# Kernel optimization log

Hardware: AMD Instinct MI355X
Metric: run time of the kernel (lower is better)

## Reference

```python
import jax, jax.numpy as jnp
import numpy as np

H = 32        # hiddenSize
OUT = 256     # output_size
T = 60        # num_frames
EPS = 1e-5


def setup_inputs() -> dict:
    key = jax.random.key(0)
    ks = jax.random.split(key, 16)
    s = 0.05
    rn = lambda k, shp: (jax.random.normal(k, shp, dtype=jnp.float32) * s)
    return {
        "x": jax.random.normal(ks[0], (1, T, 63), dtype=jnp.float32),
        "w00": rn(ks[1], (63, 63)), "b00": rn(ks[2], (63,)),
        "w01": rn(ks[3], (64, 63)), "b01": rn(ks[4], (64,)),
        "ln_g": jnp.ones((64,), jnp.float32), "ln_b": jnp.zeros((64,), jnp.float32),
        "w_ih": rn(ks[5], (4 * H, 64)), "w_hh": rn(ks[6], (4 * H, H)),
        "b_ih": rn(ks[7], (4 * H,)), "b_hh": rn(ks[8], (4 * H,)),
        "bn_g": jnp.ones((H,), jnp.float32), "bn_b": jnp.zeros((H,), jnp.float32),
        "w10": rn(ks[9], (32, H)), "b10": rn(ks[10], (32,)),
        "w11": rn(ks[11], (32, 32)), "b11": rn(ks[12], (32,)),
        "w12": rn(ks[13], (OUT, 32)), "b12": rn(ks[14], (OUT,)),
    }


def _forward(x, w00, b00, w01, b01, ln_g, ln_b, w_ih, w_hh, b_ih, b_hh,
             bn_g, bn_b, w10, b10, w11, b11, w12, b12):
    # x: [1, T, 63] -> scan over T frames (fused MLP + LayerNorm + LSTM cell)
    xs = jnp.transpose(x, (1, 0, 2))  # [T, 1, 63]

    def step(carry, xt):  # xt: [1, 63]
        h, c = carry
        f = jax.nn.relu(xt @ w00.T + b00)          # [1, 63]
        f = jax.nn.relu(f @ w01.T + b01)           # [1, 64]
        mu = jnp.mean(f, axis=-1, keepdims=True)
        var = jnp.mean((f - mu) ** 2, axis=-1, keepdims=True)
        f = (f - mu) * jax.lax.rsqrt(var + EPS) * ln_g + ln_b
        gates = f @ w_ih.T + b_ih + h @ w_hh.T + b_hh  # [1, 4H]
        i_g, f_g, g_g, o_g = jnp.split(gates, 4, axis=-1)
        c = jax.nn.sigmoid(f_g) * c + jax.nn.sigmoid(i_g) * jnp.tanh(g_g)
        h = jax.nn.sigmoid(o_g) * jnp.tanh(c)
        return (h, c), None

    h0 = jnp.zeros((1, H), x.dtype)
    c0 = jnp.zeros((1, H), x.dtype)
    (h, _), _ = jax.lax.scan(step, (h0, c0), xs)
    # BatchNorm1d in eval mode (running_mean=0, running_var=1)
    out = h * jax.lax.rsqrt(jnp.float32(1.0) + EPS) * bn_g + bn_b
    out = jax.nn.relu(out @ w10.T + b10)
    out = jax.nn.relu(out @ w11.T + b11)
    return out @ w12.T + b12  # [1, OUT]


def reference(x, w00, b00, w01, b01, ln_g, ln_b, w_ih, w_hh, b_ih, b_hh,
              bn_g, bn_b, w10, b10, w11, b11, w12, b12):
    return _forward(x, w00, b00, w01, b01, ln_g, ln_b, w_ih, w_hh, b_ih, b_hh,
                    bn_g, bn_b, w10, b10, w11, b11, w12, b12)
```

## Files before the change

### kernel.cpp

```cpp
#include <hip/hip_runtime.h>

#define EPS 1e-5f
#define MAGIC 0x5CA9F1A6u

typedef __fp16 h2v2 __attribute__((ext_vector_type(2)));

__device__ __forceinline__ float frcp(float x) { return __builtin_amdgcn_rcpf(x); }
__device__ __forceinline__ float fsigm(float x) { return frcp(1.0f + __expf(-x)); }
__device__ __forceinline__ float ftanh(float x) {
    float e = __expf(-2.0f * x);
    return (1.0f - e) * frcp(1.0f + e);
}
__device__ __forceinline__ int rdli(int v, int k) {
    return __builtin_amdgcn_readlane(v, k);
}
__device__ __forceinline__ float rdl32(float v, int k) {
    return __int_as_float(__builtin_amdgcn_readlane(__float_as_int(v), 32 + k));
}
__device__ __forceinline__ float xhalf_sum(float x) {
#if __has_builtin(__builtin_amdgcn_permlane32_swap)
    auto r = __builtin_amdgcn_permlane32_swap(__float_as_uint(x),
                                              __float_as_uint(x), false, false);
    return __uint_as_float(r[0]) + __uint_as_float(r[1]);
#else
    return x + __shfl_xor(x, 32);
#endif
}
__device__ __forceinline__ float fdot2(h2v2 a, h2v2 b, float c) {
#if __has_builtin(__builtin_amdgcn_fdot2)
    return __builtin_amdgcn_fdot2(a, b, c, false);
#else
    return c + (float)a.x * (float)b.x + (float)a.y * (float)b.y;
#endif
}

__global__ __launch_bounds__(64) void fused_kernel(
    const float* __restrict__ x,
    const float* __restrict__ w00, const float* __restrict__ b00,
    const float* __restrict__ w01, const float* __restrict__ b01,
    const float* __restrict__ ln_g, const float* __restrict__ ln_b,
    const float* __restrict__ w_ih, const float* __restrict__ w_hh,
    const float* __restrict__ b_ih, const float* __restrict__ b_hh,
    const float* __restrict__ bn_g, const float* __restrict__ bn_b,
    const float* __restrict__ w10, const float* __restrict__ b10,
    const float* __restrict__ w11, const float* __restrict__ b11,
    const float* __restrict__ w12, const float* __restrict__ b12,
    float* __restrict__ Gx, unsigned* __restrict__ flags,
    float* __restrict__ out)
{
    __shared__ float scr[128];
    const int j = threadIdx.x;

    if (blockIdx.x < 60) {
        const int t = blockIdx.x;

        scr[j] = (j < 63) ? x[t * 63 + j] : 0.0f;
        __syncthreads();

        float f0 = 0.0f;
        if (j < 63) {
            const float* wr = w00 + j * 63;
            float acc = b00[j];
            #pragma unroll
            for (int k = 0; k < 63; k++) acc += scr[k] * wr[k];
            f0 = fmaxf(acc, 0.0f);
        }
        __syncthreads();
        scr[j] = f0;
        __syncthreads();

        float acc = b01[j];
        {
            const float* wr = w01 + j * 63;
            #pragma unroll
            for (int k = 0; k < 63; k++) acc += scr[k] * wr[k];
        }
        float f1 = fmaxf(acc, 0.0f);

        float s = f1, sq = f1 * f1;
        #pragma unroll
        for (int off = 32; off > 0; off >>= 1) {
            s  += __shfl_xor(s, off);
            sq += __shfl_xor(sq, off);
        }
        float mu  = s * (1.0f / 64.0f);
        float var = sq * (1.0f / 64.0f) - mu * mu;
        float f   = (f1 - mu) * rsqrtf(var + EPS) * ln_g[j] + ln_b[j];
        __syncthreads();
        scr[64 + j] = f;
        __syncthreads();

        float a0 = b_ih[j] + b_hh[j];
        float a1 = b_ih[j + 64] + b_hh[j + 64];
        const float* wi0 = w_ih + j * 64;
        const float* wi1 = w_ih + (j + 64) * 64;
        #pragma unroll
        for (int k = 0; k < 64; k++) {
            float fk = scr[64 + k];
            a0 += fk * wi0[k];
            a1 += fk * wi1[k];
        }
        Gx[t * 128 + j]      = a0;
        Gx[t * 128 + 64 + j] = a1;

        __threadfence();
        __syncthreads();
        if (j == 0)
            __hip_atomic_store(&flags[t], MAGIC, __ATOMIC_RELEASE,
                               __HIP_MEMORY_SCOPE_AGENT);
        return;
    }

    h2v2 wAh[16], wBh[16];
    {
        const float4* r0 = (const float4*)(w_hh + j * 32);
        const float4* r1 = (const float4*)(w_hh + (j + 64) * 32);
        #pragma unroll
        for (int q = 0; q < 8; q++) {
            float4 a = r0[q];
            float4 b = r1[q];
            wAh[2 * q + 0] = __builtin_amdgcn_cvt_pkrtz(a.x, a.y);
            wAh[2 * q + 1] = __builtin_amdgcn_cvt_pkrtz(a.z, a.w);
            wBh[2 * q + 0] = __builtin_amdgcn_cvt_pkrtz(b.x, b.y);
            wBh[2 * q + 1] = __builtin_amdgcn_cvt_pkrtz(b.z, b.w);
        }
    }

    {
        bool done = (j >= 60);
        while (true) {
            if (!done)
                done = (__hip_atomic_load(&flags[j], __ATOMIC_RELAXED,
                                          __HIP_MEMORY_SCOPE_AGENT) == MAGIC);
            if (__ballot(done) == ~0ULL) break;
            __builtin_amdgcn_s_sleep(1);
        }
        (void)__hip_atomic_load(&flags[0], __ATOMIC_ACQUIRE,
                                __HIP_MEMORY_SCOPE_AGENT);
    }

    const bool low = (j < 32);
    float c = 0.0f, hn = 0.0f;
    #pragma unroll 1
    for (int c0 = 0; c0 < 5; c0++) {
        float gAr[12], gBr[12];
        #pragma unroll
        for (int i = 0; i < 12; i++) {
            gAr[i] = Gx[(c0 * 12 + i) * 128 + j];
            gBr[i] = Gx[(c0 * 12 + i) * 128 + 64 + j];
        }
        #pragma unroll
        for (int i = 0; i < 12; i++) {
            int   hsw_i = __builtin_amdgcn_update_dpp(
                              0, __float_as_int(hn), 0xB1, 0xF, 0xF, true);
            h2v2  hpk   = __builtin_amdgcn_cvt_pkrtz(hn, __int_as_float(hsw_i));
            int   hpk_i = __builtin_bit_cast(int, hpk);

            int hh_i[16];
            #pragma unroll
            for (int k = 0; k < 16; k++) hh_i[k] = rdli(hpk_i, 32 + 2 * k);

            float aA0 = gAr[i], aA1 = 0.f, aA2 = 0.f, aA3 = 0.f;
            float aB0 = gBr[i], aB1 = 0.f, aB2 = 0.f, aB3 = 0.f;
            #pragma unroll
            for (int d = 0; d < 4; d++) {
                h2v2 h0 = __builtin_bit_cast(h2v2, hh_i[d]);
                h2v2 h1 = __builtin_bit_cast(h2v2, hh_i[4 + d]);
                h2v2 hx = __builtin_bit_cast(h2v2, hh_i[8 + d]);
                h2v2 h3 = __builtin_bit_cast(h2v2, hh_i[12 + d]);
                aA0 = fdot2(h0, wAh[d],      aA0);  aB0 = fdot2(h0, wBh[d],      aB0);
                aA1 = fdot2(h1, wAh[4 + d],  aA1);  aB1 = fdot2(h1, wBh[4 + d],  aB1);
                aA2 = fdot2(hx, wAh[8 + d],  aA2);  aB2 = fdot2(hx, wBh[8 + d],  aB2);
                aA3 = fdot2(h3, wAh[12 + d], aA3);  aB3 = fdot2(h3, wBh[12 + d], aB3);
            }
            float a0 = (aA0 + aA1) + (aA2 + aA3);
            float a1 = (aB0 + aB1) + (aB2 + aB3);

            float e1 = __expf(-a1);
            float sO = frcp(1.0f + e1);
            float e2 = e1 * e1;
            float t1 = (1.0f - e2) * frcp(1.0f + e2);
            float s0 = fsigm(a0);
            float own = s0 * (low ? t1 : c);
            c = xhalf_sum(own);
            hn = sO * ftanh(c);
        }
    }

    const float rs = rsqrtf(1.0f + EPS);
    const int ro = j & 31;
    float acc = b10[ro];
    #pragma unroll
    for (int k = 0; k < 32; k++) {
        float hkk = rdl32(hn, k);
        float hb = hkk * rs * bn_g[k] + bn_b[k];
        acc += w10[ro * 32 + k] * hb;
    }
    float o1 = fmaxf(acc, 0.0f);

    acc = b11[ro];
    #pragma unroll
    for (int k = 0; k < 32; k++)
        acc += w11[ro * 32 + k]
             * __int_as_float(__builtin_amdgcn_readlane(__float_as_int(o1), k));
    float o2 = fmaxf(acc, 0.0f);

    float a[4];
    #pragma unroll
    for (int r = 0; r < 4; r++) a[r] = b12[j + 64 * r];
    #pragma unroll
    for (int k = 0; k < 32; k++) {
        float hv = __int_as_float(__builtin_amdgcn_readlane(__float_as_int(o2), k));
        #pragma unroll
        for (int r = 0; r < 4; r++) a[r] += w12[(j + 64 * r) * 32 + k] * hv;
    }
    #pragma unroll
    for (int r = 0; r < 4; r++) out[j + 64 * r] = a[r];
}

extern "C" void kernel_launch(void* const* d_in, const int* in_sizes, int n_in,
                              void* d_out, int out_size, void* d_ws, size_t ws_size,
                              hipStream_t stream) {
    const float* x    = (const float*)d_in[0];
    const float* w00  = (const float*)d_in[1];
    const float* b00  = (const float*)d_in[2];
    const float* w01  = (const float*)d_in[3];
    const float* b01  = (const float*)d_in[4];
    const float* ln_g = (const float*)d_in[5];
    const float* ln_b = (const float*)d_in[6];
    const float* w_ih = (const float*)d_in[7];
    const float* w_hh = (const float*)d_in[8];
    const float* b_ih = (const float*)d_in[9];
    const float* b_hh = (const float*)d_in[10];
    const float* bn_g = (const float*)d_in[11];
    const float* bn_b = (const float*)d_in[12];
    const float* w10  = (const float*)d_in[13];
    const float* b10  = (const float*)d_in[14];
    const float* w11  = (const float*)d_in[15];
    const float* b11  = (const float*)d_in[16];
    const float* w12  = (const float*)d_in[17];
    const float* b12  = (const float*)d_in[18];
    float* out = (float*)d_out;
    float*    Gx    = (float*)d_ws;
    unsigned* flags = (unsigned*)((char*)d_ws + 49152);

    fused_kernel<<<61, 64, 0, stream>>>(x, w00, b00, w01, b01, ln_g, ln_b,
                                        w_ih, w_hh, b_ih, b_hh, bn_g, bn_b,
                                        w10, b10, w11, b11, w12, b12,
                                        Gx, flags, out);
}
```

Before: 109.0 us.

## Wait per 12-step chunk, prefetch head weights, fold log2e into gate preactivations

The recurrent block now waits only for the flags of the current 12-frame chunk instead of all 60, so the LSTM recurrence can start while producer blocks are still computing later frame projections. The head MLP weights and biases are preloaded into registers before the recurrence, taking their global loads off the tail of the kernel. Gate preactivations and recurrent weights are prescaled by log2(e) so sigmoid and tanh use exp2 directly, and the dot-product accumulation uses 8 independent chains. Costs are higher register pressure (about 160 extra floats per lane, which may spill) and fp16 rounding of the scaled weights.

```diff
diff --git a/kernel.cpp b/kernel.cpp
--- a/kernel.cpp
+++ b/kernel.cpp
@@ -2,14 +2,17 @@
 
 #define EPS 1e-5f
 #define MAGIC 0x5CA9F1A6u
+#define LOG2E 1.44269504f
 
 typedef __fp16 h2v2 __attribute__((ext_vector_type(2)));
 
 __device__ __forceinline__ float frcp(float x) { return __builtin_amdgcn_rcpf(x); }
-__device__ __forceinline__ float fsigm(float x) { return frcp(1.0f + __expf(-x)); }
-__device__ __forceinline__ float ftanh(float x) {
-    float e = __expf(-2.0f * x);
-    return (1.0f - e) * frcp(1.0f + e);
+__device__ __forceinline__ float fexp2(float x) {
+#if __has_builtin(__builtin_amdgcn_exp2f)
+    return __builtin_amdgcn_exp2f(x);
+#else
+    return exp2f(x);
+#endif
 }
 __device__ __forceinline__ int rdli(int v, int k) {
     return __builtin_amdgcn_readlane(v, k);
@@ -100,8 +103,8 @@
             a0 += fk * wi0[k];
             a1 += fk * wi1[k];
         }
-        Gx[t * 128 + j]      = a0;
-        Gx[t * 128 + 64 + j] = a1;
+        Gx[t * 128 + j]      = a0 * LOG2E;
+        Gx[t * 128 + 64 + j] = a1 * LOG2E;
 
         __threadfence();
         __syncthreads();
@@ -119,30 +122,59 @@
         for (int q = 0; q < 8; q++) {
             float4 a = r0[q];
             float4 b = r1[q];
-            wAh[2 * q + 0] = __builtin_amdgcn_cvt_pkrtz(a.x, a.y);
-            wAh[2 * q + 1] = __builtin_amdgcn_cvt_pkrtz(a.z, a.w);
-            wBh[2 * q + 0] = __builtin_amdgcn_cvt_pkrtz(b.x, b.y);
-            wBh[2 * q + 1] = __builtin_amdgcn_cvt_pkrtz(b.z, b.w);
-        }
-    }
-
+            wAh[2 * q + 0] = __builtin_amdgcn_cvt_pkrtz(a.x * LOG2E, a.y * LOG2E);
+            wAh[2 * q + 1] = __builtin_amdgcn_cvt_pkrtz(a.z * LOG2E, a.w * LOG2E);
+            wBh[2 * q + 0] = __builtin_amdgcn_cvt_pkrtz(b.x * LOG2E, b.y * LOG2E);
+            wBh[2 * q + 1] = __builtin_amdgcn_cvt_pkrtz(b.z * LOG2E, b.w * LOG2E);
+        }
+    }
+
+    const int ro = j & 31;
+    float w10r[32], w11r[32], w12r[4][32];
+    float b10r, b11r, b12r[4];
     {
-        bool done = (j >= 60);
-        while (true) {
-            if (!done)
-                done = (__hip_atomic_load(&flags[j], __ATOMIC_RELAXED,
-                                          __HIP_MEMORY_SCOPE_AGENT) == MAGIC);
-            if (__ballot(done) == ~0ULL) break;
-            __builtin_amdgcn_s_sleep(1);
-        }
-        (void)__hip_atomic_load(&flags[0], __ATOMIC_ACQUIRE,
-                                __HIP_MEMORY_SCOPE_AGENT);
-    }
+        const float4* p10 = (const float4*)(w10 + ro * 32);
+        const float4* p11 = (const float4*)(w11 + ro * 32);
+        #pragma unroll
+        for (int q = 0; q < 8; q++) {
+            float4 a = p10[q];
+            w10r[4*q] = a.x; w10r[4*q+1] = a.y; w10r[4*q+2] = a.z; w10r[4*q+3] = a.w;
+            float4 b = p11[q];
+            w11r[4*q] = b.x; w11r[4*q+1] = b.y; w11r[4*q+2] = b.z; w11r[4*q+3] = b.w;
+        }
+        #pragma unroll
+        for (int r = 0; r < 4; r++) {
+            const float4* p12 = (const float4*)(w12 + (j + 64 * r) * 32);
+            #pragma unroll
+            for (int q = 0; q < 8; q++) {
+                float4 v = p12[q];
+                w12r[r][4*q] = v.x; w12r[r][4*q+1] = v.y;
+                w12r[r][4*q+2] = v.z; w12r[r][4*q+3] = v.w;
+            }
+            b12r[r] = b12[j + 64 * r];
+        }
+        b10r = b10[ro];
+        b11r = b11[ro];
+    }
+    float bngr = bn_g[ro], bnbr = bn_b[ro];
 
     const bool low = (j < 32);
     float c = 0.0f, hn = 0.0f;
     #pragma unroll 1
     for (int c0 = 0; c0 < 5; c0++) {
+        {
+            bool done = (j >= 12);
+            while (true) {
+                if (!done)
+                    done = (__hip_atomic_load(&flags[12 * c0 + j],
+                                              __ATOMIC_RELAXED,
+                                              __HIP_MEMORY_SCOPE_AGENT) == MAGIC);
+                if (__ballot(done) == ~0ULL) break;
+                __builtin_amdgcn_s_sleep(1);
+            }
+            (void)__hip_atomic_load(&flags[12 * c0], __ATOMIC_ACQUIRE,
+                                    __HIP_MEMORY_SCOPE_AGENT);
+        }
         float gAr[12], gBr[12];
         #pragma unroll
         for (int i = 0; i < 12; i++) {
@@ -160,59 +192,63 @@
             #pragma unroll
             for (int k = 0; k < 16; k++) hh_i[k] = rdli(hpk_i, 32 + 2 * k);
 
-            float aA0 = gAr[i], aA1 = 0.f, aA2 = 0.f, aA3 = 0.f;
-            float aB0 = gBr[i], aB1 = 0.f, aB2 = 0.f, aB3 = 0.f;
-            #pragma unroll
-            for (int d = 0; d < 4; d++) {
-                h2v2 h0 = __builtin_bit_cast(h2v2, hh_i[d]);
-                h2v2 h1 = __builtin_bit_cast(h2v2, hh_i[4 + d]);
-                h2v2 hx = __builtin_bit_cast(h2v2, hh_i[8 + d]);
-                h2v2 h3 = __builtin_bit_cast(h2v2, hh_i[12 + d]);
-                aA0 = fdot2(h0, wAh[d],      aA0);  aB0 = fdot2(h0, wBh[d],      aB0);
-                aA1 = fdot2(h1, wAh[4 + d],  aA1);  aB1 = fdot2(h1, wBh[4 + d],  aB1);
-                aA2 = fdot2(hx, wAh[8 + d],  aA2);  aB2 = fdot2(hx, wBh[8 + d],  aB2);
-                aA3 = fdot2(h3, wAh[12 + d], aA3);  aB3 = fdot2(h3, wBh[12 + d], aB3);
+            float aA[8], aB[8];
+            aA[0] = gAr[i]; aB[0] = gBr[i];
+            #pragma unroll
+            for (int q = 1; q < 8; q++) { aA[q] = 0.f; aB[q] = 0.f; }
+            #pragma unroll
+            for (int d = 0; d < 2; d++) {
+                #pragma unroll
+                for (int q = 0; q < 8; q++) {
+                    h2v2 hv = __builtin_bit_cast(h2v2, hh_i[d * 8 + q]);
+                    aA[q] = fdot2(hv, wAh[d * 8 + q], aA[q]);
+                    aB[q] = fdot2(hv, wBh[d * 8 + q], aB[q]);
+                }
             }
-            float a0 = (aA0 + aA1) + (aA2 + aA3);
-            float a1 = (aB0 + aB1) + (aB2 + aB3);
-
-            float e1 = __expf(-a1);
+            float a0 = ((aA[0]+aA[1]) + (aA[2]+aA[3]))
+                     + ((aA[4]+aA[5]) + (aA[6]+aA[7]));
+            float a1 = ((aB[0]+aB[1]) + (aB[2]+aB[3]))
+                     + ((aB[4]+aB[5]) + (aB[6]+aB[7]));
+
+            float e1 = fexp2(-a1);
             float sO = frcp(1.0f + e1);
             float e2 = e1 * e1;
             float t1 = (1.0f - e2) * frcp(1.0f + e2);
-            float s0 = fsigm(a0);
+            float s0 = frcp(1.0f + fexp2(-a0));
             float own = s0 * (low ? t1 : c);
             c = xhalf_sum(own);
-            hn = sO * ftanh(c);
+            float ec = fexp2(c * (-2.0f * LOG2E));
+            hn = sO * ((1.0f - ec) * frcp(1.0f + ec));
         }
     }
 
     const float rs = rsqrtf(1.0f + EPS);
-    const int ro = j & 31;
-    float acc = b10[ro];
+    float acc = b10r;
     #pragma unroll
     for (int k = 0; k < 32; k++) {
         float hkk = rdl32(hn, k);
-        float hb = hkk * rs * bn_g[k] + bn_b[k];
-        acc += w10[ro * 32 + k] * hb;
+        float gk = __int_as_float(rdli(__float_as_int(bngr), k));
+        float bk = __int_as_float(rdli(__float_as_int(bnbr), k));
+        float hb = hkk * rs * gk + bk;
+        acc += w10r[k] * hb;
     }
     float o1 = fmaxf(acc, 0.0f);
 
-    acc = b11[ro];
+    acc = b11r;
     #pragma unroll
     for (int k = 0; k < 32; k++)
-        acc += w11[ro * 32 + k]
+        acc += w11r[k]
              * __int_as_float(__builtin_amdgcn_readlane(__float_as_int(o1), k));
     float o2 = fmaxf(acc, 0.0f);
 
     float a[4];
     #pragma unroll
-    for (int r = 0; r < 4; r++) a[r] = b12[j + 64 * r];
+    for (int r = 0; r < 4; r++) a[r] = b12r[r];
     #pragma unroll
     for (int k = 0; k < 32; k++) {
         float hv = __int_as_float(__builtin_amdgcn_readlane(__float_as_int(o2), k));
         #pragma unroll
-        for (int r = 0; r < 4; r++) a[r] += w12[(j + 64 * r) * 32 + k] * hv;
+        for (int r = 0; r < 4; r++) a[r] += w12r[r][k] * hv;
     }
     #pragma unroll
     for (int r = 0; r < 4; r++) out[j + 64 * r] = a[r];
```

New measurement: 109.1 us. Within noise of the previous version (+0.1%).
